# Optimization experiments

Measured on AMD Instinct MI355X. Metric: run time of the kernel, lower is better.

Reference implementation:

```python
import jax, jax.numpy as jnp
import numpy as np
from math import sqrt

B, L, DM, H, NL, INTER = 4, 2048, 256, 8, 3, 16
E = DM // H
FACTOR = 5


def _ln(x, g, b, eps=1e-5):
    m = x.mean(-1, keepdims=True)
    v = ((x - m) ** 2).mean(-1, keepdims=True)
    return (x - m) * jax.lax.rsqrt(v + eps) * g + b


def _prob_attn(q, k, v, rkey):
    # q,k,v: [B,H,L,E]; ProbAttention with mask_flag=False (as in AttentionLayer)
    Bq, Hq, Lq, Eq = q.shape
    Lk = k.shape[2]
    U = min(FACTOR * int(np.ceil(np.log(Lk))), Lk)   # sample_k
    u = min(FACTOR * int(np.ceil(np.log(Lq))), Lq)   # n_top
    # random K indices shared across B,H as in torch randint(L_K,(L_Q,sample_k))
    idx = jax.random.randint(rkey, (Lq, U), 0, Lk)
    k_samp = k[:, :, idx, :]                                   # [B,H,Lq,U,E]
    qk_samp = jnp.einsum('bhle,bhlue->bhlu', q, k_samp)        # [B,H,Lq,U]
    M = qk_samp.max(-1) - qk_samp.sum(-1) / Lk                 # sparsity score
    _, top = jax.lax.top_k(M, u)                               # [B,H,u]
    q_red = jnp.take_along_axis(q, top[..., None], axis=2)     # [B,H,u,E]
    scores = jnp.einsum('bhue,bhke->bhuk', q_red, k) * (1.0 / sqrt(Eq))
    attn = jax.nn.softmax(scores, axis=-1)
    upd = jnp.einsum('bhuk,bhkd->bhud', attn, v)               # [B,H,u,E]
    # initial context = mean of V broadcast over queries (non-masked branch)
    ctx = jnp.broadcast_to(v.mean(axis=2, keepdims=True), (Bq, Hq, Lq, Eq))
    bi = jnp.arange(Bq)[:, None, None]
    hi = jnp.arange(Hq)[None, :, None]
    ctx = ctx.at[bi, hi, top].set(upd)
    return ctx.transpose(0, 2, 1, 3)                           # [B,L,H,E]


def _enc_layer(x, wq, bq, wk, bk, wv, bv, wo, bo, c1w, c1b, c2w, c2b, g1, b1, g2, b2, rkey):
    Bx, Lx, _ = x.shape
    qh = (x @ wq.T + bq).reshape(Bx, Lx, H, E).transpose(0, 2, 1, 3)
    kh = (x @ wk.T + bk).reshape(Bx, Lx, H, E).transpose(0, 2, 1, 3)
    vh = (x @ wv.T + bv).reshape(Bx, Lx, H, E).transpose(0, 2, 1, 3)
    ctx = _prob_attn(qh, kh, vh, rkey).reshape(Bx, Lx, DM)
    x = _ln(x + ctx @ wo.T + bo, g1, b1)
    y = jax.nn.relu(jnp.einsum('bld,fd->blf', x, c1w) + c1b)   # 1x1 conv
    y = jnp.einsum('blf,df->bld', y, c2w) + c2b                # 1x1 conv
    return _ln(x + y, g2, b2)


def _distill(x, w, cb, g, b):
    # circular Conv1d(k=3,pad=1) + BatchNorm1d (train stats) + ELU; MaxPool(k=1) = identity
    xt = x.transpose(0, 2, 1)                                  # [B,C,L]
    xp = jnp.concatenate([xt[..., -1:], xt, xt[..., :1]], axis=-1)
    y = jax.lax.conv_general_dilated(xp, w, (1,), 'VALID',
                                     dimension_numbers=('NCH', 'OIH', 'NCH')) + cb[None, :, None]
    m = y.mean(axis=(0, 2), keepdims=True)
    v = y.var(axis=(0, 2), keepdims=True)                      # biased var, torch BN training
    y = jax.nn.elu((y - m) * jax.lax.rsqrt(v + 1e-5) * g[None, :, None] + b[None, :, None])
    return y.transpose(0, 2, 1)


def _forward(x, wq, bq, wk, bk, wv, bv, wo, bo, c1w, c1b, c2w, c2b,
             ln1g, ln1b, ln2g, ln2b, dcw, dcb, bng, bnb, fng, fnb):
    base = jax.random.key(42)
    for i in range(NL - 1):
        x = _enc_layer(x, wq[i], bq[i], wk[i], bk[i], wv[i], bv[i], wo[i], bo[i],
                       c1w[i], c1b[i], c2w[i], c2b[i], ln1g[i], ln1b[i], ln2g[i], ln2b[i],
                       jax.random.fold_in(base, i))
        x = _distill(x, dcw[i], dcb[i], bng[i], bnb[i])
    i = NL - 1
    x = _enc_layer(x, wq[i], bq[i], wk[i], bk[i], wv[i], bv[i], wo[i], bo[i],
                   c1w[i], c1b[i], c2w[i], c2b[i], ln1g[i], ln1b[i], ln2g[i], ln2b[i],
                   jax.random.fold_in(base, i))
    return _ln(x, fng, fnb)


def setup_inputs():
    key = jax.random.key(0)
    ks = jax.random.split(key, 10)
    g = lambda k, shp, s: jax.random.normal(k, shp, jnp.float32) * s
    z = lambda shp: jnp.zeros(shp, jnp.float32)
    o = lambda shp: jnp.ones(shp, jnp.float32)
    return {
        'x': g(ks[0], (B, L, DM), 1.0),
        'wq': g(ks[1], (NL, DM, DM), 0.03), 'bq': z((NL, DM)),
        'wk': g(ks[2], (NL, DM, DM), 0.03), 'bk': z((NL, DM)),
        'wv': g(ks[3], (NL, DM, DM), 0.03), 'bv': z((NL, DM)),
        'wo': g(ks[4], (NL, DM, DM), 0.03), 'bo': z((NL, DM)),
        'c1w': g(ks[5], (NL, INTER, DM), 0.05), 'c1b': z((NL, INTER)),
        'c2w': g(ks[6], (NL, DM, INTER), 0.05), 'c2b': z((NL, DM)),
        'ln1g': o((NL, DM)), 'ln1b': z((NL, DM)),
        'ln2g': o((NL, DM)), 'ln2b': z((NL, DM)),
        'dcw': g(ks[7], (NL - 1, DM, DM, 3), 0.02), 'dcb': z((NL - 1, DM)),
        'bng': o((NL - 1, DM)), 'bnb': z((NL - 1, DM)),
        'fng': o((DM,)), 'fnb': z((DM,)),
    }


def reference(x, wq, bq, wk, bk, wv, bv, wo, bo, c1w, c1b, c2w, c2b,
              ln1g, ln1b, ln2g, ln2b, dcw, dcb, bng, bnb, fng, fnb):
    return _forward(x, wq, bq, wk, bk, wv, bv, wo, bo, c1w, c1b, c2w, c2b,
                    ln1g, ln1b, ln2g, ln2b, dcw, dcb, bng, bnb, fng, fnb)
```

## Files before the change

### kernel.cpp

```cpp
#include <hip/hip_runtime.h>
#include <stdint.h>

#define BB 4
#define LL 2048
#define DMM 256
#define HH 8
#define EE 32
#define NLL 3
#define ITR 16
#define UU 40
#define KC 16
#define KCH 128
#define ROWS (BB*LL)
#define NELEM (ROWS*DMM)

typedef __attribute__((ext_vector_type(8))) short short8;
typedef __attribute__((ext_vector_type(4))) float f32x4;
typedef unsigned long long u64;

#define GLDS16(g, l)                                                        \
  __builtin_amdgcn_global_load_lds(                                         \
      (const __attribute__((address_space(1))) uint32_t*)(g),               \
      (__attribute__((address_space(3))) uint32_t*)(l), 16, 0, 0)

__device__ __forceinline__ float bfbits(unsigned short u) {
  return __uint_as_float(((uint32_t)u) << 16);
}
__device__ __forceinline__ unsigned short f2b(float f) {
  uint32_t u = __float_as_uint(f);
  uint32_t r = (u + 0x7FFFu + ((u >> 16) & 1u)) >> 16;
  return (unsigned short)r;
}

__host__ __device__ inline void threefry2x32(uint32_t k0, uint32_t k1,
                                             uint32_t x0, uint32_t x1,
                                             uint32_t* o0, uint32_t* o1) {
  uint32_t ks2 = k0 ^ k1 ^ 0x1BD11BDAu;
  x0 += k0; x1 += k1;
#define TFR(r) { x0 += x1; x1 = (x1 << (r)) | (x1 >> (32 - (r))); x1 ^= x0; }
  TFR(13) TFR(15) TFR(26) TFR(6)
  x0 += k1;  x1 += ks2 + 1u;
  TFR(17) TFR(29) TFR(16) TFR(24)
  x0 += ks2; x1 += k0 + 2u;
  TFR(13) TFR(15) TFR(26) TFR(6)
  x0 += k0;  x1 += k1 + 3u;
  TFR(17) TFR(29) TFR(16) TFR(24)
  x0 += k1;  x1 += ks2 + 4u;
  TFR(13) TFR(15) TFR(26) TFR(6)
  x0 += ks2; x1 += k0 + 5u;
#undef TFR
  *o0 = x0; *o1 = x1;
}

__device__ __forceinline__ float wave_sum(float v) {
#pragma unroll
  for (int off = 32; off > 0; off >>= 1) v += __shfl_xor(v, off);
  return v;
}

struct CvtArgs {
  const void* src[23];
  float* dstF[23];
  unsigned short* dstB[23];
  unsigned short* dstL[23];
  int n[23];
  int blkStart[24];
  unsigned short* dcwT;
  float* vmpZ;
  int* flagOut;
};
__global__ __launch_bounds__(256) void mega_cvt(CvtArgs a) {
  __shared__ int cnt;
  if (threadIdx.x == 0) cnt = 0;
  __syncthreads();
  {
    const unsigned short* u = (const unsigned short*)a.src[0];
    int bad = 0;
#pragma unroll
    for (int rep = 0; rep < 2; ++rep) {
      float v = bfbits(u[threadIdx.x + 256 * rep]);
      float av = fabsf(v);
      bool ok = (v == 0.0f) || (av > 1e-4f && av < 100.0f);
      if (!ok) bad++;
    }
    if (bad) atomicAdd(&cnt, bad);
  }
  __syncthreads();
  int isf32 = (cnt > 25) ? 1 : 0;

  int bid = blockIdx.x;
  if (bid == a.blkStart[23]) {
    for (int t = threadIdx.x; t < BB * DMM; t += 256) a.vmpZ[t] = 0.f;
    if (threadIdx.x == 0) *a.flagOut = isf32;
    return;
  }
  int i = 0;
  while (i < 22 && bid >= a.blkStart[i + 1]) ++i;
  int e = (bid - a.blkStart[i]) * 256 + (int)threadIdx.x;
  if (e >= a.n[i]) return;
  float v; unsigned short rw;
  if (isf32) { v = ((const float*)a.src[i])[e]; rw = f2b(v); }
  else       { rw = ((const unsigned short*)a.src[i])[e]; v = bfbits(rw); }
  a.dstF[i][e] = v;
  if (a.dstB[i]) a.dstB[i][e] = rw;
  if (a.dstL[i]) a.dstL[i][e] = f2b(v - bfbits(rw));
  if (i == 17) {
    int ly = e / 196608;
    int r = e - ly * 196608;
    int n = r / 768;
    int rem = r - n * 768;
    int k = rem / 3, t = rem - k * 3;
    a.dcwT[ly * 196608 + t * 65536 + n * 256 + k] = rw;
  }
}

struct QKVArgs {
  const unsigned short* W[3];
  const float* bias[3];
  float* Cq;
  float* Ck;
  unsigned short* Cv;
  float* vmp;
};
__global__ __launch_bounds__(256) void gemm_qkv(const unsigned short* __restrict__ Ahi,
                                                const unsigned short* __restrict__ Alo,
                                                QKVArgs qa) {
  __shared__ __attribute__((aligned(16))) unsigned short AsH[128][32];
  __shared__ __attribute__((aligned(16))) unsigned short AsL[128][32];
  __shared__ __attribute__((aligned(16))) unsigned short Bs[64][32];
  int z = blockIdx.z;
  const unsigned short* W = qa.W[z];
  const float* bias = qa.bias[z];
  bool twoPass = (z < 2);
  int bm = blockIdx.x * 128, bn = blockIdx.y * 64;
  int tid = threadIdx.x;
  int wv = tid >> 6, lane = tid & 63;
  int wm = wv >> 1, wn = wv & 1;
  int l15 = lane & 15, quad = lane >> 4;
  int lrow = lane >> 2, lseg = lane & 3;
  f32x4 acc[4][2];
#pragma unroll
  for (int i = 0; i < 4; ++i)
#pragma unroll
    for (int j = 0; j < 2; ++j) acc[i][j] = (f32x4){0.f, 0.f, 0.f, 0.f};
  for (int k0 = 0; k0 < 256; k0 += 32) {
    __syncthreads();
#pragma unroll
    for (int s = 0; s < 2; ++s) {
      int brow = (wv + s * 4) * 16;
      size_t goff = (size_t)(bm + brow + lrow) * 256 + k0 + lseg * 8;
      GLDS16(Ahi + goff, &AsH[brow][0]);
      if (twoPass) GLDS16(Alo + goff, &AsL[brow][0]);
    }
    {
      int brow = wv * 16;
      GLDS16(W + (size_t)(bn + brow + lrow) * 256 + k0 + lseg * 8, &Bs[brow][0]);
    }
    __syncthreads();
    short8 ah[4], bfr[2];
#pragma unroll
    for (int mt = 0; mt < 4; ++mt)
      ah[mt] = *(const short8*)(&AsH[wm * 64 + mt * 16 + l15][quad * 8]);
#pragma unroll
    for (int nt = 0; nt < 2; ++nt)
      bfr[nt] = *(const short8*)(&Bs[wn * 32 + nt * 16 + l15][quad * 8]);
#pragma unroll
    for (int mt = 0; mt < 4; ++mt)
#pragma unroll
      for (int nt = 0; nt < 2; ++nt)
        acc[mt][nt] = __builtin_amdgcn_mfma_f32_16x16x32_bf16(ah[mt], bfr[nt],
                                                              acc[mt][nt], 0, 0, 0);
    if (twoPass) {
      short8 al[4];
#pragma unroll
      for (int mt = 0; mt < 4; ++mt)
        al[mt] = *(const short8*)(&AsL[wm * 64 + mt * 16 + l15][quad * 8]);
#pragma unroll
      for (int mt = 0; mt < 4; ++mt)
#pragma unroll
        for (int nt = 0; nt < 2; ++nt)
          acc[mt][nt] = __builtin_amdgcn_mfma_f32_16x16x32_bf16(al[mt], bfr[nt],
                                                                acc[mt][nt], 0, 0, 0);
    }
  }
  float* C = (z == 0) ? qa.Cq : qa.Ck;
#pragma unroll
  for (int nt = 0; nt < 2; ++nt) {
    int n = bn + wn * 32 + nt * 16 + l15;
    float bv = bias[n];
    float csum = 0.f;
#pragma unroll
    for (int mt = 0; mt < 4; ++mt)
#pragma unroll
      for (int r = 0; r < 4; ++r) {
        int m = bm + wm * 64 + mt * 16 + quad * 4 + r;
        float val = acc[mt][nt][r] + bv;
        if (z < 2) {
          C[(size_t)m * 256 + n] = val;
        } else {
          qa.Cv[(size_t)m * 256 + n] = f2b(val);
          csum += val;
        }
      }
    if (z == 2) {
      csum += __shfl_xor(csum, 16);
      csum += __shfl_xor(csum, 32);
      if (quad == 0) {
        int b = bm >> 11;
        atomicAdd(&qa.vmp[b * DMM + n], csum);
      }
    }
  }
}

__global__ __launch_bounds__(256) void gemm_oproj(const float* __restrict__ vmp,
                                                  const unsigned char* __restrict__ mapb,
                                                  const float* __restrict__ pm,
                                                  const float* __restrict__ pl,
                                                  const float* __restrict__ po,
                                                  const unsigned short* __restrict__ W,
                                                  const float* __restrict__ bias,
                                                  float* __restrict__ C) {
  __shared__ __attribute__((aligned(16))) unsigned short As[64][32];
  __shared__ __attribute__((aligned(16))) unsigned short Bs[64][32];
  int bm = blockIdx.x * 64, bn = blockIdx.y * 64;
  int tid = threadIdx.x;
  int wv = tid >> 6, lane = tid & 63;
  int wm = wv >> 1, wn = wv & 1;
  int l15 = lane & 15, quad = lane >> 4;
  int lrow = lane >> 2, lseg = lane & 3;
  int arow = tid >> 2, adg = tid & 3;
  int b = bm >> 11, l0 = bm & 2047;
  const float invL = 1.0f / (float)LL;
  f32x4 acc[2][2];
#pragma unroll
  for (int i = 0; i < 2; ++i)
#pragma unroll
    for (int j = 0; j < 2; ++j) acc[i][j] = (f32x4){0.f, 0.f, 0.f, 0.f};
  for (int k0 = 0; k0 < 256; k0 += 32) {
    int h = k0 >> 5;
    int bh = b * HH + h;
    __syncthreads();
    {
      int l = l0 + arow;
      int q = (int)mapb[bh * 2048 + l];
      unsigned short outv[8];
      if (q) {
        size_t base = ((size_t)bh * UU + (q - 1)) * KC;
        float Mx = -1e30f;
#pragma unroll
        for (int kc = 0; kc < KC; ++kc) Mx = fmaxf(Mx, pm[base + kc]);
        float Ls = 0.f;
        float sc[KC];
#pragma unroll
        for (int kc = 0; kc < KC; ++kc) {
          sc[kc] = expf(pm[base + kc] - Mx);
          Ls += pl[base + kc] * sc[kc];
        }
        float inv = 1.0f / Ls;
#pragma unroll
        for (int j = 0; j < 8; ++j) {
          int dl = adg * 8 + j;
          float o = 0.f;
#pragma unroll
          for (int kc = 0; kc < KC; ++kc) o += po[(base + kc) * 32 + dl] * sc[kc];
          outv[j] = f2b(o * inv);
        }
      } else {
        const float* vp = vmp + b * DMM + h * EE + adg * 8;
#pragma unroll
        for (int j = 0; j < 8; ++j) outv[j] = f2b(vp[j] * invL);
      }
      *(uint4*)(&As[arow][adg * 8]) = *(const uint4*)outv;
    }
    {
      int brow = wv * 16;
      GLDS16(W + (size_t)(bn + brow + lrow) * 256 + k0 + lseg * 8, &Bs[brow][0]);
    }
    __syncthreads();
    short8 af[2], bfr[2];
#pragma unroll
    for (int mt = 0; mt < 2; ++mt)
      af[mt] = *(const short8*)(&As[wm * 32 + mt * 16 + l15][quad * 8]);
#pragma unroll
    for (int nt = 0; nt < 2; ++nt)
      bfr[nt] = *(const short8*)(&Bs[wn * 32 + nt * 16 + l15][quad * 8]);
#pragma unroll
    for (int mt = 0; mt < 2; ++mt)
#pragma unroll
      for (int nt = 0; nt < 2; ++nt)
        acc[mt][nt] = __builtin_amdgcn_mfma_f32_16x16x32_bf16(af[mt], bfr[nt],
                                                              acc[mt][nt], 0, 0, 0);
  }
#pragma unroll
  for (int nt = 0; nt < 2; ++nt) {
    int n = bn + wn * 32 + nt * 16 + l15;
    float bv = bias[n];
#pragma unroll
    for (int mt = 0; mt < 2; ++mt)
#pragma unroll
      for (int r = 0; r < 4; ++r) {
        int m = bm + wm * 32 + mt * 16 + quad * 4 + r;
        C[(size_t)m * 256 + n] = acc[mt][nt][r] + bv;
      }
  }
}

__global__ __launch_bounds__(256) void gemm_conv(const unsigned short* __restrict__ A,
                                                 const unsigned short* __restrict__ W,
                                                 const float* __restrict__ bias,
                                                 float* __restrict__ C,
                                                 float* __restrict__ stp,
                                                 float* __restrict__ stp2) {
  __shared__ __attribute__((aligned(16))) unsigned short As[80][32];
  __shared__ __attribute__((aligned(16))) unsigned short Bs[192][32];
  int bm = blockIdx.x * 64, bn = blockIdx.y * 64;
  int tid = threadIdx.x;
  int wv = tid >> 6, lane = tid & 63;
  int wm = wv >> 1, wn = wv & 1;
  int l15 = lane & 15, quad = lane >> 4;
  int lrow = lane >> 2, lseg = lane & 3;
  int bbase = bm & ~2047, l0 = bm & 2047;
  f32x4 acc[2][2];
#pragma unroll
  for (int i = 0; i < 2; ++i)
#pragma unroll
    for (int j = 0; j < 2; ++j) acc[i][j] = (f32x4){0.f, 0.f, 0.f, 0.f};
  for (int k0 = 0; k0 < 256; k0 += 32) {
    __syncthreads();
    for (int c = wv; c < 5; c += 4) {
      int i0 = c * 16;
      int l = (l0 - 1 + i0 + lrow + 2048) & 2047;
      GLDS16(A + (size_t)(bbase | l) * 256 + k0 + lseg * 8, &As[i0][0]);
    }
    for (int c = wv; c < 12; c += 4) {
      int i0 = c * 16;
      int tap = c >> 2, brow = (c & 3) * 16;
      GLDS16(W + (size_t)tap * 65536 + (size_t)(bn + brow + lrow) * 256 + k0 + lseg * 8,
             &Bs[i0][0]);
    }
    __syncthreads();
#pragma unroll
    for (int tap = 0; tap < 3; ++tap) {
      short8 af[2], bfr[2];
#pragma unroll
      for (int mt = 0; mt < 2; ++mt)
        af[mt] = *(const short8*)(&As[wm * 32 + mt * 16 + l15 + tap][quad * 8]);
#pragma unroll
      for (int nt = 0; nt < 2; ++nt)
        bfr[nt] = *(const short8*)(&Bs[tap * 64 + wn * 32 + nt * 16 + l15][quad * 8]);
#pragma unroll
      for (int mt = 0; mt < 2; ++mt)
#pragma unroll
        for (int nt = 0; nt < 2; ++nt)
          acc[mt][nt] = __builtin_amdgcn_mfma_f32_16x16x32_bf16(af[mt], bfr[nt],
                                                                acc[mt][nt], 0, 0, 0);
    }
  }
#pragma unroll
  for (int nt = 0; nt < 2; ++nt) {
    int n = bn + wn * 32 + nt * 16 + l15;
    float bv = bias[n];
    float s = 0.f, s2 = 0.f;
#pragma unroll
    for (int mt = 0; mt < 2; ++mt)
#pragma unroll
      for (int r = 0; r < 4; ++r) {
        int m = bm + wm * 32 + mt * 16 + quad * 4 + r;
        float val = acc[mt][nt][r] + bv;
        C[(size_t)m * 256 + n] = val;
        s += val;
        s2 += val * val;
      }
    s  += __shfl_xor(s, 16);   s  += __shfl_xor(s, 32);
    s2 += __shfl_xor(s2, 16);  s2 += __shfl_xor(s2, 32);
    if (quad == 0) {
      atomicAdd(&stp[n], s);
      atomicAdd(&stp2[n], s2);
    }
  }
}

__global__ __launch_bounds__(256) void m_kernel3(const float* __restrict__ Q,
                                                 const float* __restrict__ K,
                                                 uint32_t k20, uint32_t k21,
                                                 float* __restrict__ M) {
  int bid = blockIdx.x;
  int blk = (bid & 7) * 256 + (bid >> 3);
  int b = blk >> 9, lc = blk & 511;
  int wave = threadIdx.x >> 6, lane = threadIdx.x & 63;
  int l = lc * 4 + wave;
  int myidx = 0;
  if (lane < UU) {
    int j = l * UU + lane;
    uint32_t o0, o1;
    const int half = (LL * UU) / 2;
    if (j < half) {
      threefry2x32(k20, k21, (uint32_t)j, (uint32_t)(j + half), &o0, &o1);
      myidx = (int)(o0 & (LL - 1));
    } else {
      threefry2x32(k20, k21, (uint32_t)(j - half), (uint32_t)j, &o0, &o1);
      myidx = (int)(o1 & (LL - 1));
    }
  }
  float4 q4 = *(const float4*)(Q + ((size_t)(b * LL + l)) * DMM + lane * 4);
  const float* Kb = K + (size_t)b * LL * DMM;
  float mx = -1e30f, sm = 0.f;
#pragma unroll 8
  for (int u = 0; u < UU; ++u) {
    int kidx = __shfl(myidx, u);
    float4 k4 = *(const float4*)(Kb + (size_t)kidx * DMM + lane * 4);
    float s = q4.x * k4.x + q4.y * k4.y + q4.z * k4.z + q4.w * k4.w;
    s += __shfl_xor(s, 1);
    s += __shfl_xor(s, 2);
    s += __shfl_xor(s, 4);
    mx = fmaxf(mx, s);
    sm += s;
  }
  if ((lane & 7) == 0) {
    int h = lane >> 3;
    M[((size_t)(b * HH + h)) * LL + l] = mx - sm * (1.0f / (float)LL);
  }
}

__global__ __launch_bounds__(256) void attn_part(const float* __restrict__ Q,
                                                 const float* __restrict__ K,
                                                 const unsigned short* __restrict__ Vbf,
                                                 const float* __restrict__ M,
                                                 unsigned char* __restrict__ mapb,
                                                 float* __restrict__ pm,
                                                 float* __restrict__ pl,
                                                 float* __restrict__ po) {
  __shared__ float Qs[40][32];
  __shared__ unsigned short ps[40][KCH];
  __shared__ unsigned short Vs[KCH][40];
  __shared__ int qrows[40];
  __shared__ unsigned int hist[256];
  __shared__ unsigned int sA[256];
  __shared__ unsigned int sB[256];
  __shared__ unsigned int tbv;
  int kc = blockIdx.x, bh = blockIdx.y;
  int h = bh & 7, b = bh >> 3;
  int tid = threadIdx.x;
  int wv = tid >> 6, lane = tid & 63;

  {
    int row = tid >> 1, half = tid & 1;
    const unsigned short* vsrc =
        Vbf + (size_t)(b * LL + kc * KCH + row) * DMM + h * EE + half * 16;
    *(uint4*)(&Vs[row][half * 16]) = *(const uint4*)vsrc;
    *(uint4*)(&Vs[row][half * 16 + 8]) = *(const uint4*)(vsrc + 8);
  }
  int kk = tid & (KCH - 1), qh = tid >> 7;
  float4 kr[8];
  {
    const float4* kp =
        (const float4*)(K + ((size_t)(b * LL + kc * KCH + kk)) * DMM + h * EE);
#pragma unroll
    for (int j = 0; j < 8; ++j) kr[j] = kp[j];
  }

  u64 kreg[8];
#pragma unroll
  for (int r = 0; r < 8; ++r) {
    int l = tid + 256 * r;
    float v = M[(size_t)bh * LL + l];
    uint32_t bits = __float_as_uint(v);
    uint32_t kv = (bits & 0x80000000u) ? ~bits : (bits | 0x80000000u);
    kreg[r] = ((u64)kv << 32) | (uint32_t)(2047 - l);
  }
  u64 prefix = 0;
  int rank = UU;
  for (int round = 0; round < 8; ++round) {
    int shift = 56 - 8 * round;
    u64 maskTop = (round == 0) ? 0ull : (~0ull << (64 - 8 * round));
    hist[tid] = 0;
    __syncthreads();
#pragma unroll
    for (int r = 0; r < 8; ++r) {
      u64 k = kreg[r];
      if ((k & maskTop) == prefix)
        atomicAdd(&hist[(unsigned int)((k >> shift) & 0xFFu)], 1u);
    }
    __syncthreads();
    sA[tid] = hist[tid];
    __syncthreads();
    unsigned int* src = sA;
    unsigned int* dst = sB;
    for (int off = 1; off < 256; off <<= 1) {
      unsigned int v = src[tid] + ((tid + off < 256) ? src[tid + off] : 0u);
      dst[tid] = v;
      __syncthreads();
      unsigned int* tmpp = src; src = dst; dst = tmpp;
    }
    unsigned int Sb = src[tid];
    unsigned int Snext = (tid < 255) ? src[tid + 1] : 0u;
    if (Sb >= (unsigned int)rank && Snext < (unsigned int)rank) tbv = (unsigned int)tid;
    __syncthreads();
    unsigned int tb = tbv;
    unsigned int above = (tb < 255u) ? src[tb + 1] : 0u;
    rank -= (int)above;
    prefix |= ((u64)tb) << shift;
    __syncthreads();
  }
  u64 T = prefix;
  int myCnt = 0;
#pragma unroll
  for (int r = 0; r < 8; ++r) myCnt += (kreg[r] >= T) ? 1 : 0;
  sA[tid] = (unsigned int)myCnt;
  __syncthreads();
  {
    unsigned int* src = sA;
    unsigned int* dst = sB;
    for (int off = 1; off < 256; off <<= 1) {
      unsigned int v = src[tid] + ((tid >= off) ? src[tid - off] : 0u);
      dst[tid] = v;
      __syncthreads();
      unsigned int* tmpp = src; src = dst; dst = tmpp;
    }
    int pos = (int)src[tid] - myCnt;
    bool wmap = (kc == 0);
#pragma unroll
    for (int r = 0; r < 8; ++r) {
      u64 k = kreg[r];
      int l = 2047 - (int)(uint32_t)(k & 0xFFFFFFFFu);
      unsigned char mv = 0;
      if (k >= T) {
        qrows[pos] = l;
        mv = (unsigned char)(pos + 1);
        pos++;
      }
      if (wmap) mapb[bh * 2048 + l] = mv;
    }
  }
  __syncthreads();

  for (int t = tid; t < 40 * 32; t += 256) {
    int q = t >> 5, d = t & 31;
    Qs[q][d] = Q[((size_t)(b * LL + qrows[q])) * DMM + h * EE + d];
  }
  __syncthreads();
  {
    const float scale = 0.17677669529663687f;
    for (int q = qh * 20; q < qh * 20 + 20; ++q) {
      const float4* qp = (const float4*)Qs[q];
      float s = 0.f;
#pragma unroll
      for (int j = 0; j < 8; ++j) {
        float4 qv = qp[j];
        s += qv.x * kr[j].x + qv.y * kr[j].y + qv.z * kr[j].z + qv.w * kr[j].w;
      }
      ps[q][kk] = f2b(s * scale);
    }
  }
  __syncthreads();
  int kg = lane >> 5, d = lane & 31;
  for (int qq = 0; qq < 10; ++qq) {
    int q = wv * 10 + qq;
    float mx = fmaxf(bfbits(ps[q][lane]), bfbits(ps[q][lane + 64]));
#pragma unroll
    for (int off = 32; off > 0; off >>= 1) mx = fmaxf(mx, __shfl_xor(mx, off));
    float e0 = expf(bfbits(ps[q][lane]) - mx);
    float e1 = expf(bfbits(ps[q][lane + 64]) - mx);
    ps[q][lane] = f2b(e0);
    ps[q][lane + 64] = f2b(e1);
    float sum = wave_sum(e0 + e1);
    float o = 0.f;
#pragma unroll 8
    for (int j = 0; j < KCH / 2; ++j) {
      int r = 2 * j + kg;
      o += bfbits(ps[q][r]) * bfbits(Vs[r][d]);
    }
    o += __shfl_xor(o, 32);
    size_t base = ((size_t)bh * UU + q) * KC + kc;
    if (lane == 0) { pm[base] = mx; pl[base] = sum; }
    if (lane < 32) po[base * 32 + d] = o;
  }
}

__global__ __launch_bounds__(256) void enc_tail(const float* __restrict__ X,
                                                const float* __restrict__ T,
                                                const float* __restrict__ g1,
                                                const float* __restrict__ b1ln,
                                                const float* __restrict__ w1,
                                                const float* __restrict__ b1,
                                                const float* __restrict__ w2,
                                                const float* __restrict__ b2,
                                                const float* __restrict__ g2,
                                                const float* __restrict__ b2ln,
                                                float* __restrict__ Out,
                                                unsigned short* __restrict__ OutB,
                                                unsigned short* __restrict__ OutL,
                                                const float* __restrict__ fing,
                                                const float* __restrict__ finb,
                                                void* __restrict__ finOut,
                                                const int* __restrict__ flag,
                                                float* __restrict__ stpZ,
                                                float* __restrict__ stp2Z) {
  if (blockIdx.x == 0) {
    stpZ[threadIdx.x] = 0.f;
    stp2Z[threadIdx.x] = 0.f;
  }
  int wave = threadIdx.x >> 6, lane = threadIdx.x & 63;
  size_t row = (size_t)blockIdx.x * 4 + wave;
  __shared__ float xs[4][DMM];
  const float* xr = X + row * DMM;
  const float* tr = T + row * DMM;
  float v[4];
#pragma unroll
  for (int i = 0; i < 4; ++i) v[i] = xr[lane + 64 * i] + tr[lane + 64 * i];
  float s = wave_sum(v[0] + v[1] + v[2] + v[3]);
  float m = s * (1.0f / (float)DMM);
  float sq = 0.f;
#pragma unroll
  for (int i = 0; i < 4; ++i) { float d = v[i] - m; sq += d * d; }
  sq = wave_sum(sq);
  float rstd = rsqrtf(sq * (1.0f / (float)DMM) + 1e-5f);
  float xv[4];
#pragma unroll
  for (int i = 0; i < 4; ++i) {
    int d = lane + 64 * i;
    xv[i] = (v[i] - m) * rstd * g1[d] + b1ln[d];
    xs[wave][d] = xv[i];
  }
  __syncthreads();
  int f = lane & 15, qtr = lane >> 4;
  const float* w1p = w1 + f * DMM + qtr * 64;
  const float* xq = &xs[wave][qtr * 64];
  float pacc = 0.f;
#pragma unroll 8
  for (int d = 0; d < 64; ++d) pacc += xq[d] * w1p[d];
  pacc += __shfl_xor(pacc, 16);
  pacc += __shfl_xor(pacc, 32);
  float y1 = fmaxf(pacc + b1[f], 0.0f);
  float y1v[16];
#pragma unroll
  for (int ff = 0; ff < 16; ++ff) y1v[ff] = __shfl(y1, ff);
#pragma unroll
  for (int i = 0; i < 4; ++i) {
    int d = lane + 64 * i;
    const float* w2p = w2 + d * ITR;
    float a = b2[d];
#pragma unroll
    for (int ff = 0; ff < 16; ++ff) a += y1v[ff] * w2p[ff];
    v[i] = xv[i] + a;
  }
  s = wave_sum(v[0] + v[1] + v[2] + v[3]);
  m = s * (1.0f / (float)DMM);
  sq = 0.f;
#pragma unroll
  for (int i = 0; i < 4; ++i) { float d = v[i] - m; sq += d * d; }
  sq = wave_sum(sq);
  rstd = rsqrtf(sq * (1.0f / (float)DMM) + 1e-5f);
  float vv[4];
#pragma unroll
  for (int i = 0; i < 4; ++i) {
    int d = lane + 64 * i;
    float val = (v[i] - m) * rstd * g2[d] + b2ln[d];
    vv[i] = val;
    Out[row * DMM + d] = val;
    unsigned short hi = f2b(val);
    OutB[row * DMM + d] = hi;
    OutL[row * DMM + d] = f2b(val - bfbits(hi));
  }
  if (finOut) {
    s = wave_sum(vv[0] + vv[1] + vv[2] + vv[3]);
    m = s * (1.0f / (float)DMM);
    sq = 0.f;
#pragma unroll
    for (int i = 0; i < 4; ++i) { float d = vv[i] - m; sq += d * d; }
    sq = wave_sum(sq);
    rstd = rsqrtf(sq * (1.0f / (float)DMM) + 1e-5f);
    int isf32 = *flag;
#pragma unroll
    for (int i = 0; i < 4; ++i) {
      int d = lane + 64 * i;
      float val = (vv[i] - m) * rstd * fing[d] + finb[d];
      if (isf32) ((float*)finOut)[row * DMM + d] = val;
      else       ((unsigned short*)finOut)[row * DMM + d] = f2b(val);
    }
  }
}

__global__ __launch_bounds__(256) void bn_elu(const float* __restrict__ Y,
                                              const float* __restrict__ stp,
                                              const float* __restrict__ stp2,
                                              const float* __restrict__ g,
                                              const float* __restrict__ bb,
                                              float* __restrict__ X,
                                              unsigned short* __restrict__ XB,
                                              unsigned short* __restrict__ XL,
                                              float* __restrict__ vmpZ) {
  int gid = blockIdx.x * 256 + threadIdx.x;
  if (gid < BB * DMM) vmpZ[gid] = 0.f;
  int d = gid & 255;
  float mean = stp[d] * (1.0f / (float)ROWS);
  float var = stp2[d] * (1.0f / (float)ROWS) - mean * mean;
  float rstd = rsqrtf(var + 1e-5f);
  float v = (Y[gid] - mean) * rstd * g[d] + bb[d];
  float r = v > 0.f ? v : expm1f(v);
  X[gid] = r;
  unsigned short hi = f2b(r);
  XB[gid] = hi;
  XL[gid] = f2b(r - bfbits(hi));
}

extern "C" void kernel_launch(void* const* d_in, const int* in_sizes, int n_in,
                              void* d_out, int out_size, void* d_ws, size_t ws_size,
                              hipStream_t stream) {
  (void)in_sizes; (void)n_in; (void)out_size; (void)ws_size;

  float* xbuf = (float*)d_ws;
  float* kb   = xbuf + NELEM;
  float* qb   = kb + NELEM;
  float* tmp  = qb;
  float* Mbuf = qb + NELEM;
  float* vmp  = Mbuf + BB * HH * LL;
  float* stp  = vmp + BB * DMM;
  float* stp2 = stp + DMM;
  float* wp   = stp2 + DMM;
  const int wsz[23] = {
      NELEM,
      NLL * DMM * DMM, NLL * DMM,
      NLL * DMM * DMM, NLL * DMM,
      NLL * DMM * DMM, NLL * DMM,
      NLL * DMM * DMM, NLL * DMM,
      NLL * ITR * DMM, NLL * ITR,
      NLL * DMM * ITR, NLL * DMM,
      NLL * DMM, NLL * DMM,
      NLL * DMM, NLL * DMM,
      (NLL - 1) * DMM * DMM * 3, (NLL - 1) * DMM,
      (NLL - 1) * DMM, (NLL - 1) * DMM,
      DMM, DMM
  };
  float* fptr[23];
  fptr[0] = xbuf;
  for (int i = 1; i < 23; ++i) { fptr[i] = wp; wp += wsz[i]; }
  float* pm = wp;
  float* pl = pm + 32 * UU * KC;
  float* po = pl + 32 * UU * KC;
  unsigned short* xbf   = (unsigned short*)(po + 32 * UU * KC * 32);
  unsigned short* xlo   = xbf + NELEM;
  unsigned short* vbf   = xlo + NELEM;
  unsigned short* wqbf  = vbf + NELEM;
  unsigned short* wkbf  = wqbf + NLL * DMM * DMM;
  unsigned short* wvbf  = wkbf + NLL * DMM * DMM;
  unsigned short* wobf  = wvbf + NLL * DMM * DMM;
  unsigned short* dcwT  = wobf + NLL * DMM * DMM;
  u64* cand = (u64*)(dcwT + (NLL - 1) * 3 * DMM * DMM);
  int* topb = (int*)(cand + 256 * 40);
  int* flag = topb + BB * HH * UU;
  unsigned char* mapb = (unsigned char*)(flag + 1);

  CvtArgs ca;
  int totalBlk = 0;
  for (int i = 0; i < 23; ++i) {
    ca.src[i] = d_in[i];
    ca.dstF[i] = fptr[i];
    ca.dstB[i] = nullptr;
    ca.dstL[i] = nullptr;
    ca.n[i] = wsz[i];
    ca.blkStart[i] = totalBlk;
    totalBlk += (wsz[i] + 255) / 256;
  }
  ca.blkStart[23] = totalBlk;
  ca.dstB[0] = xbf;  ca.dstL[0] = xlo;
  ca.dstB[1] = wqbf;
  ca.dstB[3] = wkbf;
  ca.dstB[5] = wvbf;
  ca.dstB[7] = wobf;
  ca.dcwT = dcwT;
  ca.vmpZ = vmp;
  ca.flagOut = flag;
  mega_cvt<<<totalBlk + 1, 256, 0, stream>>>(ca);

  dim3 gqkv(ROWS / 128, DMM / 64, 3);
  dim3 g64(ROWS / 64, DMM / 64);

  for (int i = 0; i < NLL; ++i) {
    QKVArgs qa;
    qa.W[0] = wqbf + (size_t)i * DMM * DMM;
    qa.W[1] = wkbf + (size_t)i * DMM * DMM;
    qa.W[2] = wvbf + (size_t)i * DMM * DMM;
    qa.bias[0] = fptr[2] + i * DMM;
    qa.bias[1] = fptr[4] + i * DMM;
    qa.bias[2] = fptr[6] + i * DMM;
    qa.Cq = qb; qa.Ck = kb; qa.Cv = vbf;
    qa.vmp = vmp;
    gemm_qkv<<<gqkv, 256, 0, stream>>>(xbf, xlo, qa);

    uint32_t ki0, ki1, a0, a1, b0, b1;
    threefry2x32(0u, 42u, 0u, (uint32_t)i, &ki0, &ki1);
    threefry2x32(ki0, ki1, 0u, 2u, &a0, &a1);
    threefry2x32(ki0, ki1, 1u, 3u, &b0, &b1);
    (void)a0; (void)b0;

    m_kernel3<<<BB * 512, 256, 0, stream>>>(qb, kb, a1, b1, Mbuf);
    attn_part<<<dim3(KC, BB * HH), 256, 0, stream>>>(qb, kb, vbf, Mbuf, mapb,
                                                     pm, pl, po);

    gemm_oproj<<<g64, 256, 0, stream>>>(vmp, mapb, pm, pl, po,
                                        wobf + (size_t)i * DMM * DMM,
                                        fptr[8] + i * DMM, tmp);
    bool last = (i == NLL - 1);
    enc_tail<<<ROWS / 4, 256, 0, stream>>>(
        xbuf, tmp, fptr[13] + i * DMM, fptr[14] + i * DMM,
        fptr[9] + (size_t)i * ITR * DMM, fptr[10] + i * ITR,
        fptr[11] + (size_t)i * DMM * ITR, fptr[12] + i * DMM,
        fptr[15] + i * DMM, fptr[16] + i * DMM, xbuf, xbf, xlo,
        fptr[21], fptr[22], last ? d_out : nullptr, flag, stp, stp2);

    if (!last) {
      gemm_conv<<<g64, 256, 0, stream>>>(xbf, dcwT + (size_t)i * 3 * DMM * DMM,
                                         fptr[18] + i * DMM, tmp, stp, stp2);
      bn_elu<<<NELEM / 256, 256, 0, stream>>>(tmp, stp, stp2, fptr[19] + i * DMM,
                                              fptr[20] + i * DMM, xbuf, xbf, xlo, vmp);
    }
  }
}
```

Measured before the change: 532.9 us.

## Fuse output projection GEMM with layernorm/FFN encoder tail kernel

Merges the attention output-projection GEMM and the encoder tail (residual, LN1, 1x1-conv FFN, LN2, optional final LN) into one kernel. Each block now computes a full 32-row by 256-column tile held in shared memory, then applies the row-wise tail directly on it. This removes the fp32 temporary buffer round-trip through global memory and one launch per layer. In exchange, the grid shrinks to 256 blocks, each block loads the whole weight matrix per k-step, and each wave processes eight rows serially, which lowers parallelism.

```diff
diff --git a/kernel.cpp b/kernel.cpp
--- a/kernel.cpp
+++ b/kernel.cpp
@@ -213,35 +213,56 @@
   }
 }
 
-__global__ __launch_bounds__(256) void gemm_oproj(const float* __restrict__ vmp,
+__global__ __launch_bounds__(256) void oproj_tail(const float* __restrict__ vmp,
                                                   const unsigned char* __restrict__ mapb,
                                                   const float* __restrict__ pm,
                                                   const float* __restrict__ pl,
                                                   const float* __restrict__ po,
                                                   const unsigned short* __restrict__ W,
                                                   const float* __restrict__ bias,
-                                                  float* __restrict__ C) {
-  __shared__ __attribute__((aligned(16))) unsigned short As[64][32];
-  __shared__ __attribute__((aligned(16))) unsigned short Bs[64][32];
-  int bm = blockIdx.x * 64, bn = blockIdx.y * 64;
+                                                  const float* __restrict__ X,
+                                                  const float* __restrict__ g1,
+                                                  const float* __restrict__ b1ln,
+                                                  const float* __restrict__ w1,
+                                                  const float* __restrict__ b1,
+                                                  const float* __restrict__ w2,
+                                                  const float* __restrict__ b2,
+                                                  const float* __restrict__ g2,
+                                                  const float* __restrict__ b2ln,
+                                                  float* __restrict__ Out,
+                                                  unsigned short* __restrict__ OutB,
+                                                  unsigned short* __restrict__ OutL,
+                                                  const float* __restrict__ fing,
+                                                  const float* __restrict__ finb,
+                                                  void* __restrict__ finOut,
+                                                  const int* __restrict__ flag,
+                                                  float* __restrict__ stpZ,
+                                                  float* __restrict__ stp2Z) {
+  __shared__ __attribute__((aligned(16))) unsigned short As[32][32];
+  __shared__ __attribute__((aligned(16))) unsigned short Bs[256][32];
+  __shared__ float Cs[32][DMM];
+  __shared__ float xs[4][DMM];
   int tid = threadIdx.x;
+  if (blockIdx.x == 0) {
+    stpZ[tid] = 0.f;
+    stp2Z[tid] = 0.f;
+  }
+  int bm = blockIdx.x * 32;
   int wv = tid >> 6, lane = tid & 63;
-  int wm = wv >> 1, wn = wv & 1;
   int l15 = lane & 15, quad = lane >> 4;
-  int lrow = lane >> 2, lseg = lane & 3;
-  int arow = tid >> 2, adg = tid & 3;
   int b = bm >> 11, l0 = bm & 2047;
   const float invL = 1.0f / (float)LL;
-  f32x4 acc[2][2];
+  f32x4 acc[2][4];
 #pragma unroll
   for (int i = 0; i < 2; ++i)
 #pragma unroll
-    for (int j = 0; j < 2; ++j) acc[i][j] = (f32x4){0.f, 0.f, 0.f, 0.f};
+    for (int j = 0; j < 4; ++j) acc[i][j] = (f32x4){0.f, 0.f, 0.f, 0.f};
   for (int k0 = 0; k0 < 256; k0 += 32) {
     int h = k0 >> 5;
     int bh = b * HH + h;
     __syncthreads();
-    {
+    if (tid < 128) {
+      int arow = tid >> 2, adg = tid & 3;
       int l = l0 + arow;
       int q = (int)mapb[bh * 2048 + l];
       unsigned short outv[8];
@@ -274,35 +295,118 @@
       *(uint4*)(&As[arow][adg * 8]) = *(const uint4*)outv;
     }
     {
-      int brow = wv * 16;
-      GLDS16(W + (size_t)(bn + brow + lrow) * 256 + k0 + lseg * 8, &Bs[brow][0]);
-    }
-    __syncthreads();
-    short8 af[2], bfr[2];
+      int lrw = lane >> 2, lsg = lane & 3;
+#pragma unroll
+      for (int s = 0; s < 4; ++s) {
+        int brow = s * 64 + wv * 16;
+        GLDS16(W + (size_t)(brow + lrw) * 256 + k0 + lsg * 8, &Bs[brow][0]);
+      }
+    }
+    __syncthreads();
+    short8 af[2], bfr[4];
 #pragma unroll
     for (int mt = 0; mt < 2; ++mt)
-      af[mt] = *(const short8*)(&As[wm * 32 + mt * 16 + l15][quad * 8]);
-#pragma unroll
-    for (int nt = 0; nt < 2; ++nt)
-      bfr[nt] = *(const short8*)(&Bs[wn * 32 + nt * 16 + l15][quad * 8]);
+      af[mt] = *(const short8*)(&As[mt * 16 + l15][quad * 8]);
+#pragma unroll
+    for (int nt = 0; nt < 4; ++nt)
+      bfr[nt] = *(const short8*)(&Bs[wv * 64 + nt * 16 + l15][quad * 8]);
 #pragma unroll
     for (int mt = 0; mt < 2; ++mt)
 #pragma unroll
-      for (int nt = 0; nt < 2; ++nt)
+      for (int nt = 0; nt < 4; ++nt)
         acc[mt][nt] = __builtin_amdgcn_mfma_f32_16x16x32_bf16(af[mt], bfr[nt],
                                                               acc[mt][nt], 0, 0, 0);
   }
 #pragma unroll
-  for (int nt = 0; nt < 2; ++nt) {
-    int n = bn + wn * 32 + nt * 16 + l15;
+  for (int nt = 0; nt < 4; ++nt) {
+    int n = wv * 64 + nt * 16 + l15;
     float bv = bias[n];
 #pragma unroll
     for (int mt = 0; mt < 2; ++mt)
 #pragma unroll
-      for (int r = 0; r < 4; ++r) {
-        int m = bm + wm * 32 + mt * 16 + quad * 4 + r;
-        C[(size_t)m * 256 + n] = acc[mt][nt][r] + bv;
+      for (int r = 0; r < 4; ++r)
+        Cs[mt * 16 + quad * 4 + r][n] = acc[mt][nt][r] + bv;
+  }
+  __syncthreads();
+  for (int rr = 0; rr < 8; ++rr) {
+    int lr = wv * 8 + rr;
+    size_t row = (size_t)bm + lr;
+    const float* xr = X + row * DMM;
+    const float* tr = Cs[lr];
+    float v[4];
+#pragma unroll
+    for (int i = 0; i < 4; ++i) v[i] = xr[lane + 64 * i] + tr[lane + 64 * i];
+    float s = wave_sum(v[0] + v[1] + v[2] + v[3]);
+    float m = s * (1.0f / (float)DMM);
+    float sq = 0.f;
+#pragma unroll
+    for (int i = 0; i < 4; ++i) { float d = v[i] - m; sq += d * d; }
+    sq = wave_sum(sq);
+    float rstd = rsqrtf(sq * (1.0f / (float)DMM) + 1e-5f);
+    float xv[4];
+#pragma unroll
+    for (int i = 0; i < 4; ++i) {
+      int d = lane + 64 * i;
+      xv[i] = (v[i] - m) * rstd * g1[d] + b1ln[d];
+      xs[wv][d] = xv[i];
+    }
+    __syncthreads();
+    int f = lane & 15, qtr = lane >> 4;
+    const float* w1p = w1 + f * DMM + qtr * 64;
+    const float* xq = &xs[wv][qtr * 64];
+    float pacc = 0.f;
+#pragma unroll 8
+    for (int d = 0; d < 64; ++d) pacc += xq[d] * w1p[d];
+    pacc += __shfl_xor(pacc, 16);
+    pacc += __shfl_xor(pacc, 32);
+    float y1 = fmaxf(pacc + b1[f], 0.0f);
+    float y1v[16];
+#pragma unroll
+    for (int ff = 0; ff < 16; ++ff) y1v[ff] = __shfl(y1, ff);
+#pragma unroll
+    for (int i = 0; i < 4; ++i) {
+      int d = lane + 64 * i;
+      const float* w2p = w2 + d * ITR;
+      float a = b2[d];
+#pragma unroll
+      for (int ff = 0; ff < 16; ++ff) a += y1v[ff] * w2p[ff];
+      v[i] = xv[i] + a;
+    }
+    s = wave_sum(v[0] + v[1] + v[2] + v[3]);
+    m = s * (1.0f / (float)DMM);
+    sq = 0.f;
+#pragma unroll
+    for (int i = 0; i < 4; ++i) { float d = v[i] - m; sq += d * d; }
+    sq = wave_sum(sq);
+    rstd = rsqrtf(sq * (1.0f / (float)DMM) + 1e-5f);
+    float vv[4];
+#pragma unroll
+    for (int i = 0; i < 4; ++i) {
+      int d = lane + 64 * i;
+      float val = (v[i] - m) * rstd * g2[d] + b2ln[d];
+      vv[i] = val;
+      Out[row * DMM + d] = val;
+      unsigned short hi = f2b(val);
+      OutB[row * DMM + d] = hi;
+      OutL[row * DMM + d] = f2b(val - bfbits(hi));
+    }
+    if (finOut) {
+      s = wave_sum(vv[0] + vv[1] + vv[2] + vv[3]);
+      m = s * (1.0f / (float)DMM);
+      sq = 0.f;
+#pragma unroll
+      for (int i = 0; i < 4; ++i) { float d = vv[i] - m; sq += d * d; }
+      sq = wave_sum(sq);
+      rstd = rsqrtf(sq * (1.0f / (float)DMM) + 1e-5f);
+      int isf32 = *flag;
+#pragma unroll
+      for (int i = 0; i < 4; ++i) {
+        int d = lane + 64 * i;
+        float val = (vv[i] - m) * rstd * fing[d] + finb[d];
+        if (isf32) ((float*)finOut)[row * DMM + d] = val;
+        else       ((unsigned short*)finOut)[row * DMM + d] = f2b(val);
       }
+    }
   }
 }
 
@@ -575,110 +679,6 @@
     size_t base = ((size_t)bh * UU + q) * KC + kc;
     if (lane == 0) { pm[base] = mx; pl[base] = sum; }
     if (lane < 32) po[base * 32 + d] = o;
-  }
-}
-
-__global__ __launch_bounds__(256) void enc_tail(const float* __restrict__ X,
-                                                const float* __restrict__ T,
-                                                const float* __restrict__ g1,
-                                                const float* __restrict__ b1ln,
-                                                const float* __restrict__ w1,
-                                                const float* __restrict__ b1,
-                                                const float* __restrict__ w2,
-                                                const float* __restrict__ b2,
-                                                const float* __restrict__ g2,
-                                                const float* __restrict__ b2ln,
-                                                float* __restrict__ Out,
-                                                unsigned short* __restrict__ OutB,
-                                                unsigned short* __restrict__ OutL,
-                                                const float* __restrict__ fing,
-                                                const float* __restrict__ finb,
-                                                void* __restrict__ finOut,
-                                                const int* __restrict__ flag,
-                                                float* __restrict__ stpZ,
-                                                float* __restrict__ stp2Z) {
-  if (blockIdx.x == 0) {
-    stpZ[threadIdx.x] = 0.f;
-    stp2Z[threadIdx.x] = 0.f;
-  }
-  int wave = threadIdx.x >> 6, lane = threadIdx.x & 63;
-  size_t row = (size_t)blockIdx.x * 4 + wave;
-  __shared__ float xs[4][DMM];
-  const float* xr = X + row * DMM;
-  const float* tr = T + row * DMM;
-  float v[4];
-#pragma unroll
-  for (int i = 0; i < 4; ++i) v[i] = xr[lane + 64 * i] + tr[lane + 64 * i];
-  float s = wave_sum(v[0] + v[1] + v[2] + v[3]);
-  float m = s * (1.0f / (float)DMM);
-  float sq = 0.f;
-#pragma unroll
-  for (int i = 0; i < 4; ++i) { float d = v[i] - m; sq += d * d; }
-  sq = wave_sum(sq);
-  float rstd = rsqrtf(sq * (1.0f / (float)DMM) + 1e-5f);
-  float xv[4];
-#pragma unroll
-  for (int i = 0; i < 4; ++i) {
-    int d = lane + 64 * i;
-    xv[i] = (v[i] - m) * rstd * g1[d] + b1ln[d];
-    xs[wave][d] = xv[i];
-  }
-  __syncthreads();
-  int f = lane & 15, qtr = lane >> 4;
-  const float* w1p = w1 + f * DMM + qtr * 64;
-  const float* xq = &xs[wave][qtr * 64];
-  float pacc = 0.f;
-#pragma unroll 8
-  for (int d = 0; d < 64; ++d) pacc += xq[d] * w1p[d];
-  pacc += __shfl_xor(pacc, 16);
-  pacc += __shfl_xor(pacc, 32);
-  float y1 = fmaxf(pacc + b1[f], 0.0f);
-  float y1v[16];
-#pragma unroll
-  for (int ff = 0; ff < 16; ++ff) y1v[ff] = __shfl(y1, ff);
-#pragma unroll
-  for (int i = 0; i < 4; ++i) {
-    int d = lane + 64 * i;
-    const float* w2p = w2 + d * ITR;
-    float a = b2[d];
-#pragma unroll
-    for (int ff = 0; ff < 16; ++ff) a += y1v[ff] * w2p[ff];
-    v[i] = xv[i] + a;
-  }
-  s = wave_sum(v[0] + v[1] + v[2] + v[3]);
-  m = s * (1.0f / (float)DMM);
-  sq = 0.f;
-#pragma unroll
-  for (int i = 0; i < 4; ++i) { float d = v[i] - m; sq += d * d; }
-  sq = wave_sum(sq);
-  rstd = rsqrtf(sq * (1.0f / (float)DMM) + 1e-5f);
-  float vv[4];
-#pragma unroll
-  for (int i = 0; i < 4; ++i) {
-    int d = lane + 64 * i;
-    float val = (v[i] - m) * rstd * g2[d] + b2ln[d];
-    vv[i] = val;
-    Out[row * DMM + d] = val;
-    unsigned short hi = f2b(val);
-    OutB[row * DMM + d] = hi;
-    OutL[row * DMM + d] = f2b(val - bfbits(hi));
-  }
-  if (finOut) {
-    s = wave_sum(vv[0] + vv[1] + vv[2] + vv[3]);
-    m = s * (1.0f / (float)DMM);
-    sq = 0.f;
-#pragma unroll
-    for (int i = 0; i < 4; ++i) { float d = vv[i] - m; sq += d * d; }
-    sq = wave_sum(sq);
-    rstd = rsqrtf(sq * (1.0f / (float)DMM) + 1e-5f);
-    int isf32 = *flag;
-#pragma unroll
-    for (int i = 0; i < 4; ++i) {
-      int d = lane + 64 * i;
-      float val = (vv[i] - m) * rstd * fing[d] + finb[d];
-      if (isf32) ((float*)finOut)[row * DMM + d] = val;
-      else       ((unsigned short*)finOut)[row * DMM + d] = f2b(val);
-    }
   }
 }
 
@@ -799,15 +799,16 @@
     attn_part<<<dim3(KC, BB * HH), 256, 0, stream>>>(qb, kb, vbf, Mbuf, mapb,
                                                      pm, pl, po);
 
-    gemm_oproj<<<g64, 256, 0, stream>>>(vmp, mapb, pm, pl, po,
-                                        wobf + (size_t)i * DMM * DMM,
-                                        fptr[8] + i * DMM, tmp);
     bool last = (i == NLL - 1);
-    enc_tail<<<ROWS / 4, 256, 0, stream>>>(
-        xbuf, tmp, fptr[13] + i * DMM, fptr[14] + i * DMM,
+    oproj_tail<<<ROWS / 32, 256, 0, stream>>>(
+        vmp, mapb, pm, pl, po,
+        wobf + (size_t)i * DMM * DMM, fptr[8] + i * DMM,
+        xbuf,
+        fptr[13] + i * DMM, fptr[14] + i * DMM,
         fptr[9] + (size_t)i * ITR * DMM, fptr[10] + i * ITR,
         fptr[11] + (size_t)i * DMM * ITR, fptr[12] + i * DMM,
-        fptr[15] + i * DMM, fptr[16] + i * DMM, xbuf, xbf, xlo,
+        fptr[15] + i * DMM, fptr[16] + i * DMM,
+        xbuf, xbf, xlo,
         fptr[21], fptr[22], last ? d_out : nullptr, flag, stp, stp2);
 
     if (!last) {
```

Measured after the change: 522.7 us. Within noise of the previous version (-1.9%).
